# Kernel optimization log

Measured on AMD Instinct MI355X. Metric: run time of the kernel, lower is better.

## Reference

```python
import jax, jax.numpy as jnp
import numpy as np

B, N, C = 32, 2248, 1024
D = 128            # bottleneck (down_size)
P = 200            # num_prompt_tokens
SCALE = D ** (-0.5)


def setup_inputs() -> dict:
    key = jax.random.key(0)
    k = jax.random.split(key, 5)
    return {
        "x": jax.random.normal(k[0], (B, N, C), dtype=jnp.float32),
        "W_down": jax.random.normal(k[1], (C, D), dtype=jnp.float32) * (C ** -0.5),
        "b_down": jax.random.normal(k[2], (D,), dtype=jnp.float32) * 0.01,
        "W_up": jax.random.normal(k[3], (D, C), dtype=jnp.float32) * (D ** -0.5),
        "b_up": jax.random.normal(k[4], (C,), dtype=jnp.float32) * 0.01,
        "gate": jnp.ones((), dtype=jnp.float32),
    }


def reference(x, W_down, b_down, W_up, b_up, gate):
    # down-projection + exact GELU (torch nn.GELU default is erf-based)
    down = jax.nn.gelu(jnp.einsum('bnc,cd->bnd', x, W_down) + b_down,
                       approximate=False)                      # [B, N, D]
    prompt_down = down[:, :P, :]                               # [B, P, D]
    token_down = down[:, P:, :]                                # [B, N-P, D]
    # prompt-token cross attention
    attn = jax.nn.softmax(
        jnp.einsum('bpd,btd->bpt', prompt_down, token_down) * SCALE, axis=-1)
    prompt_out = jnp.einsum('bpt,btd->bpd', attn, token_down)  # [B, P, D]
    combined = jnp.concatenate([prompt_out, token_down], axis=1)  # [B, N, D]
    up = jnp.einsum('bnd,dc->bnc', combined, W_up) + b_up      # [B, N, C]
    return gate * up
```

## Files before the change

### kernel.cpp

```cpp
#include <hip/hip_runtime.h>
#include <hip/hip_bf16.h>
#include <math.h>

#define B_   32
#define N_   2248
#define C_   1024
#define D_   128
#define P_   200
#define T_   2048
#define M_   (B_ * N_)
#define SCALE_ 0.08838834764831845f

typedef __bf16 bf16;
typedef __bf16 bf16x8 __attribute__((ext_vector_type(8)));
typedef __bf16 bf16x4 __attribute__((ext_vector_type(4)));
typedef float  f32x4  __attribute__((ext_vector_type(4)));
typedef unsigned int u32x4 __attribute__((ext_vector_type(4)));

#define VT_COL(dd, t) ((((((t) >> 3) ^ (((dd) >> 3) & 7)) << 3)) | ((t) & 7))

__global__ void k_prep(const float* __restrict__ Wd, const float* __restrict__ Wu,
                       bf16* __restrict__ WtD, bf16* __restrict__ WtU) {
    int i = blockIdx.x * 256 + threadIdx.x;
    if (i >= 131072) return;
    int d = i >> 10, k = i & 1023;
    WtD[i] = (bf16)Wd[k * 128 + d];
    int c = i >> 7, e = i & 127;
    WtU[i] = (bf16)Wu[e * 1024 + c];
}

__launch_bounds__(256, 3)
__global__ void k_down(const float* __restrict__ x, const bf16* __restrict__ WtD,
                       const float* __restrict__ bd, bf16* __restrict__ down) {
    __shared__ bf16 As[2][128][72];
    const int tid = threadIdx.x;
    const int lane = tid & 63, wid = tid >> 6;
    const int wm = wid >> 1, wn = wid & 1;
    const int li = lane & 15, lg = lane >> 4;
    const int m0 = blockIdx.x * 128;
    const bf16* Bp = WtD + (size_t)(wn * 64 + li) * C_ + lg * 8;

    int r_[4], c_[4];
    const float* sp[4];
#pragma unroll
    for (int it = 0; it < 4; it++) {
        int ch = tid + it * 256;
        r_[it] = ch >> 3;
        c_[it] = (ch & 7) * 8;
        sp[it] = x + (size_t)(m0 + r_[it]) * C_ + c_[it];
    }

    f32x4 stg[8];
#pragma unroll
    for (int it = 0; it < 4; it++) {
        stg[2 * it]     = *(const f32x4*)(sp[it]);
        stg[2 * it + 1] = *(const f32x4*)(sp[it] + 4);
    }
#pragma unroll
    for (int it = 0; it < 4; it++) {
        bf16x8 o;
        o[0] = (bf16)stg[2*it][0]; o[1] = (bf16)stg[2*it][1];
        o[2] = (bf16)stg[2*it][2]; o[3] = (bf16)stg[2*it][3];
        o[4] = (bf16)stg[2*it+1][0]; o[5] = (bf16)stg[2*it+1][1];
        o[6] = (bf16)stg[2*it+1][2]; o[7] = (bf16)stg[2*it+1][3];
        *(bf16x8*)&As[0][r_[it]][c_[it]] = o;
    }

    f32x4 acc[4][4];
    const f32x4 zero = {0.f, 0.f, 0.f, 0.f};
#pragma unroll
    for (int i = 0; i < 4; i++)
#pragma unroll
        for (int j = 0; j < 4; j++) acc[i][j] = zero;

    int cur = 0;
    for (int t = 0; t < 16; t++) {
        __syncthreads();
        if (t < 15) {
#pragma unroll
            for (int it = 0; it < 4; it++) {
                stg[2 * it]     = *(const f32x4*)(sp[it] + (t + 1) * 64);
                stg[2 * it + 1] = *(const f32x4*)(sp[it] + (t + 1) * 64 + 4);
            }
        }
        const int k0 = t * 64;
#pragma unroll
        for (int kk = 0; kk < 2; kk++) {
            bf16x8 af[4], bf_[4];
#pragma unroll
            for (int f = 0; f < 4; f++)
                bf_[f] = *(const bf16x8*)(Bp + (size_t)(f * 16) * C_ + k0 + kk * 32);
#pragma unroll
            for (int f = 0; f < 4; f++)
                af[f] = *(const bf16x8*)&As[cur][wm * 64 + f * 16 + li][kk * 32 + lg * 8];
#pragma unroll
            for (int fm = 0; fm < 4; fm++)
#pragma unroll
                for (int fn = 0; fn < 4; fn++)
                    acc[fm][fn] = __builtin_amdgcn_mfma_f32_16x16x32_bf16(
                        af[fm], bf_[fn], acc[fm][fn], 0, 0, 0);
        }
        if (t < 15) {
#pragma unroll
            for (int it = 0; it < 4; it++) {
                bf16x8 o;
                o[0] = (bf16)stg[2*it][0]; o[1] = (bf16)stg[2*it][1];
                o[2] = (bf16)stg[2*it][2]; o[3] = (bf16)stg[2*it][3];
                o[4] = (bf16)stg[2*it+1][0]; o[5] = (bf16)stg[2*it+1][1];
                o[6] = (bf16)stg[2*it+1][2]; o[7] = (bf16)stg[2*it+1][3];
                *(bf16x8*)&As[cur ^ 1][r_[it]][c_[it]] = o;
            }
        }
        cur ^= 1;
    }
#pragma unroll
    for (int fn = 0; fn < 4; fn++) {
        int col = wn * 64 + fn * 16 + li;
        float bias = bd[col];
#pragma unroll
        for (int fm = 0; fm < 4; fm++) {
            int rb = m0 + wm * 64 + fm * 16 + lg * 4;
#pragma unroll
            for (int r = 0; r < 4; r++) {
                float v = acc[fm][fn][r] + bias;
                float g = 0.5f * v * (1.0f + erff(v * 0.70710678118654752f));
                down[(size_t)(rb + r) * D_ + col] = (bf16)g;
            }
        }
    }
}

__launch_bounds__(256, 2)
__global__ void k_attn(const bf16* __restrict__ down, float* __restrict__ Opart,
                       float* __restrict__ Mpart, float* __restrict__ Lpart) {
    __shared__ bf16 Qs[64][136];
    __shared__ bf16 Ks[64][136];
    __shared__ bf16 Vt[128][72];
    __shared__ bf16 Ps[4][16][72];
    const int tid = threadIdx.x;
    const int lane = tid & 63, w = tid >> 6;
    const int li = lane & 15, lg = lane >> 4;
    const int bid = blockIdx.x;
    const int wg = (bid & 7) * 64 + (bid >> 3);
    const int b  = wg >> 4;
    const int qt = (wg >> 2) & 3;
    const int th = wg & 3;
    const size_t base = (size_t)b * N_ * D_;
    const int tbase = P_ + th * 512;

#pragma unroll
    for (int it = 0; it < 4; it++) {
        int ch = tid + it * 256;
        int r = ch >> 4, c8 = (ch & 15) * 8;
        *(u32x4*)&Qs[r][c8] = *(const u32x4*)(down + base + (size_t)(qt * 64 + r) * D_ + c8);
    }
    __syncthreads();
    bf16x8 qf[4];
#pragma unroll
    for (int kk = 0; kk < 4; kk++)
        qf[kk] = *(const bf16x8*)&Qs[w * 16 + li][kk * 32 + lg * 8];

    float m_run[4], l_run[4];
    f32x4 acc[8];
    const f32x4 zero = {0.f, 0.f, 0.f, 0.f};
#pragma unroll
    for (int r = 0; r < 4; r++) { m_run[r] = -3.0e38f; l_run[r] = 0.f; }
#pragma unroll
    for (int fn = 0; fn < 8; fn++) acc[fn] = zero;

    for (int tt = 0; tt < 8; tt++) {
        __syncthreads();
#pragma unroll
        for (int it = 0; it < 4; it++) {
            int ch = tid + it * 256;
            int r = ch >> 4, c8 = (ch & 15) * 8;
            u32x4 v = *(const u32x4*)(down + base + (size_t)(tbase + tt * 64 + r) * D_ + c8);
            *(u32x4*)&Ks[r][c8] = v;
            bf16 tmp[8];
            *(u32x4*)tmp = v;
#pragma unroll
            for (int j = 0; j < 8; j++) Vt[c8 + j][VT_COL(c8 + j, r)] = tmp[j];
        }
        __syncthreads();
        f32x4 s[4];
#pragma unroll
        for (int fn = 0; fn < 4; fn++) {
            s[fn] = zero;
#pragma unroll
            for (int kk = 0; kk < 4; kk++) {
                bf16x8 kf = *(const bf16x8*)&Ks[fn * 16 + li][kk * 32 + lg * 8];
                s[fn] = __builtin_amdgcn_mfma_f32_16x16x32_bf16(qf[kk], kf, s[fn], 0, 0, 0);
            }
            s[fn] *= SCALE_;
        }
#pragma unroll
        for (int r = 0; r < 4; r++) {
            float tmax = fmaxf(fmaxf(s[0][r], s[1][r]), fmaxf(s[2][r], s[3][r]));
#pragma unroll
            for (int off = 1; off < 16; off <<= 1)
                tmax = fmaxf(tmax, __shfl_xor(tmax, off, 64));
            float mnew = fmaxf(m_run[r], tmax);
            float corr = __expf(m_run[r] - mnew);
            m_run[r] = mnew;
            float psum = 0.f;
#pragma unroll
            for (int fn = 0; fn < 4; fn++) {
                float p = __expf(s[fn][r] - mnew);
                psum += p;
                Ps[w][lg * 4 + r][fn * 16 + li] = (bf16)p;
            }
#pragma unroll
            for (int off = 1; off < 16; off <<= 1)
                psum += __shfl_xor(psum, off, 64);
            l_run[r] = l_run[r] * corr + psum;
#pragma unroll
            for (int fn = 0; fn < 8; fn++) acc[fn][r] *= corr;
        }
#pragma unroll
        for (int kk = 0; kk < 2; kk++) {
            bf16x8 pf = *(const bf16x8*)&Ps[w][li][kk * 32 + lg * 8];
#pragma unroll
            for (int fn = 0; fn < 8; fn++) {
                int d = fn * 16 + li;
                bf16x8 vf = *(const bf16x8*)&Vt[d][VT_COL(d, kk * 32 + lg * 8)];
                acc[fn] = __builtin_amdgcn_mfma_f32_16x16x32_bf16(pf, vf, acc[fn], 0, 0, 0);
            }
        }
    }
#pragma unroll
    for (int r = 0; r < 4; r++) {
        int q = qt * 64 + w * 16 + lg * 4 + r;
        size_t ro = ((size_t)(b * 4 + th) * 256 + q) * 128;
#pragma unroll
        for (int fn = 0; fn < 8; fn++)
            Opart[ro + fn * 16 + li] = acc[fn][r];
        if (li == 0) {
            Mpart[(b * 4 + th) * 256 + q] = m_run[r];
            Lpart[(b * 4 + th) * 256 + q] = l_run[r];
        }
    }
}

__global__ void k_comb(const float* __restrict__ Opart, const float* __restrict__ Mpart,
                       const float* __restrict__ Lpart, bf16* __restrict__ pout) {
    int gid = blockIdx.x * 256 + threadIdx.x;
    if (gid >= (B_ * P_ * D_) / 4) return;
    int e = gid * 4;
    int row = e >> 7;
    int col = e & 127;
    int b = row / P_;
    int q = row - b * P_;
    float mm[4], ll[4];
    float m = -3.0e38f;
#pragma unroll
    for (int t = 0; t < 4; t++) {
        mm[t] = Mpart[(b * 4 + t) * 256 + q];
        ll[t] = Lpart[(b * 4 + t) * 256 + q];
        m = fmaxf(m, mm[t]);
    }
    float a[4], lsum = 0.f;
#pragma unroll
    for (int t = 0; t < 4; t++) { a[t] = __expf(mm[t] - m); lsum += ll[t] * a[t]; }
    float inv = 1.0f / lsum;
    f32x4 o = {0.f, 0.f, 0.f, 0.f};
#pragma unroll
    for (int t = 0; t < 4; t++) {
        f32x4 ot = *(const f32x4*)&Opart[((size_t)(b * 4 + t) * 256 + q) * 128 + col];
#pragma unroll
        for (int j = 0; j < 4; j++) o[j] += ot[j] * a[t];
    }
    bf16x4 ob;
#pragma unroll
    for (int j = 0; j < 4; j++) ob[j] = (bf16)(o[j] * inv);
    *(bf16x4*)&pout[(size_t)row * 128 + col] = ob;
}

__launch_bounds__(256, 3)
__global__ void k_up(const bf16* __restrict__ down, const bf16* __restrict__ pout,
                     const bf16* __restrict__ WtU, const float* __restrict__ bu,
                     const float* __restrict__ gate, float* __restrict__ out) {
    const int tid = threadIdx.x;
    const int lane = tid & 63, wid = tid >> 6;
    const int wm = wid >> 1, wn = wid & 1;
    const int li = lane & 15, lg = lane >> 4;
    int bid = blockIdx.x;
    int wg = (bid & 7) * 562 + (bid >> 3);
    const int mt = wg >> 3, nt = wg & 7;
    const int m0 = mt * 128, n0 = nt * 128;

    const bf16* rp[4];
#pragma unroll
    for (int f = 0; f < 4; f++) {
        int row = m0 + wm * 64 + f * 16 + li;
        int bb = row / N_;
        int n = row - bb * N_;
        rp[f] = (n < P_) ? (pout + (size_t)(bb * P_ + n) * D_ + lg * 8)
                         : (down + (size_t)row * D_ + lg * 8);
    }
    const bf16* Bp = WtU + (size_t)(n0 + wn * 64 + li) * D_ + lg * 8;

    f32x4 acc[4][4];
    const f32x4 zero = {0.f, 0.f, 0.f, 0.f};
#pragma unroll
    for (int i = 0; i < 4; i++)
#pragma unroll
        for (int j = 0; j < 4; j++) acc[i][j] = zero;

#pragma unroll
    for (int kk = 0; kk < 4; kk++) {
        bf16x8 af[4], bf_[4];
#pragma unroll
        for (int f = 0; f < 4; f++) {
            af[f]  = *(const bf16x8*)(rp[f] + kk * 32);
            bf_[f] = *(const bf16x8*)(Bp + (size_t)(f * 16) * D_ + kk * 32);
        }
#pragma unroll
        for (int fm = 0; fm < 4; fm++)
#pragma unroll
            for (int fn = 0; fn < 4; fn++)
                acc[fm][fn] = __builtin_amdgcn_mfma_f32_16x16x32_bf16(
                    af[fm], bf_[fn], acc[fm][fn], 0, 0, 0);
    }

    float g = gate[0];
#pragma unroll
    for (int fn = 0; fn < 4; fn++) {
        int c = n0 + wn * 64 + fn * 16 + li;
        float bias = bu[c];
#pragma unroll
        for (int fm = 0; fm < 4; fm++) {
            int rb = m0 + wm * 64 + fm * 16 + lg * 4;
#pragma unroll
            for (int r = 0; r < 4; r++)
                out[(size_t)(rb + r) * C_ + c] = g * (acc[fm][fn][r] + bias);
        }
    }
}

extern "C" void kernel_launch(void* const* d_in, const int* in_sizes, int n_in,
                              void* d_out, int out_size, void* d_ws, size_t ws_size,
                              hipStream_t stream) {
    const float* x    = (const float*)d_in[0];
    const float* Wd   = (const float*)d_in[1];
    const float* bd   = (const float*)d_in[2];
    const float* Wu   = (const float*)d_in[3];
    const float* bu   = (const float*)d_in[4];
    const float* gate = (const float*)d_in[5];
    float* out = (float*)d_out;

    char* w = (char*)d_ws;
    bf16*  down  = (bf16*)w;
    bf16*  pout  = (bf16*)(w + 18415616);
    bf16*  WtD   = (bf16*)(w + 20054016);
    bf16*  WtU   = (bf16*)(w + 20316160);
    float* Opart = (float*)(w + 20578304);
    float* Mpart = (float*)(w + 37355520);
    float* Lpart = (float*)(w + 37486592);

    k_prep<<<512, 256, 0, stream>>>(Wd, Wu, WtD, WtU);
    k_down<<<M_ / 128, 256, 0, stream>>>(x, WtD, bd, down);
    k_attn<<<512, 256, 0, stream>>>(down, Opart, Mpart, Lpart);
    k_comb<<<800, 256, 0, stream>>>(Opart, Mpart, Lpart, pout);
    k_up<<<(M_ / 128) * 8, 256, 0, stream>>>(down, pout, WtU, bu, gate, out);
}
```

Before: 255.7 us.

## Retile down-projection GEMM to 64-row blocks with full-width warp N tiles

The down-projection kernel now uses 64-row M tiles with 128-wide K steps. Each warp owns 16 rows and all 128 output columns, where before a 2x2 warp grid split 64x64 tiles. The change doubles the block count, lowers per-thread accumulator registers, and raises the occupancy hint from 3 to 4. In exchange, each warp now re-reads the whole WtD slice from global/L2 per A fragment, which raises weight traffic per row.

```diff
diff --git a/kernel.cpp b/kernel.cpp
--- a/kernel.cpp
+++ b/kernel.cpp
@@ -29,24 +29,23 @@
     WtU[i] = (bf16)Wu[e * 1024 + c];
 }
 
-__launch_bounds__(256, 3)
+__launch_bounds__(256, 4)
 __global__ void k_down(const float* __restrict__ x, const bf16* __restrict__ WtD,
                        const float* __restrict__ bd, bf16* __restrict__ down) {
-    __shared__ bf16 As[2][128][72];
+    __shared__ bf16 As[2][64][136];
     const int tid = threadIdx.x;
-    const int lane = tid & 63, wid = tid >> 6;
-    const int wm = wid >> 1, wn = wid & 1;
+    const int lane = tid & 63, w = tid >> 6;
     const int li = lane & 15, lg = lane >> 4;
-    const int m0 = blockIdx.x * 128;
-    const bf16* Bp = WtD + (size_t)(wn * 64 + li) * C_ + lg * 8;
+    const int m0 = blockIdx.x * 64;
+    const bf16* Bp = WtD + (size_t)li * C_ + lg * 8;
 
     int r_[4], c_[4];
     const float* sp[4];
 #pragma unroll
     for (int it = 0; it < 4; it++) {
         int ch = tid + it * 256;
-        r_[it] = ch >> 3;
-        c_[it] = (ch & 7) * 8;
+        r_[it] = ch >> 4;
+        c_[it] = (ch & 15) * 8;
         sp[it] = x + (size_t)(m0 + r_[it]) * C_ + c_[it];
     }
 
@@ -59,53 +58,44 @@
 #pragma unroll
     for (int it = 0; it < 4; it++) {
         bf16x8 o;
-        o[0] = (bf16)stg[2*it][0]; o[1] = (bf16)stg[2*it][1];
-        o[2] = (bf16)stg[2*it][2]; o[3] = (bf16)stg[2*it][3];
+        o[0] = (bf16)stg[2*it][0];   o[1] = (bf16)stg[2*it][1];
+        o[2] = (bf16)stg[2*it][2];   o[3] = (bf16)stg[2*it][3];
         o[4] = (bf16)stg[2*it+1][0]; o[5] = (bf16)stg[2*it+1][1];
         o[6] = (bf16)stg[2*it+1][2]; o[7] = (bf16)stg[2*it+1][3];
         *(bf16x8*)&As[0][r_[it]][c_[it]] = o;
     }
 
-    f32x4 acc[4][4];
+    f32x4 acc[8];
     const f32x4 zero = {0.f, 0.f, 0.f, 0.f};
 #pragma unroll
-    for (int i = 0; i < 4; i++)
-#pragma unroll
-        for (int j = 0; j < 4; j++) acc[i][j] = zero;
+    for (int f = 0; f < 8; f++) acc[f] = zero;
 
     int cur = 0;
-    for (int t = 0; t < 16; t++) {
+    for (int t = 0; t < 8; t++) {
         __syncthreads();
-        if (t < 15) {
+        if (t < 7) {
 #pragma unroll
             for (int it = 0; it < 4; it++) {
-                stg[2 * it]     = *(const f32x4*)(sp[it] + (t + 1) * 64);
-                stg[2 * it + 1] = *(const f32x4*)(sp[it] + (t + 1) * 64 + 4);
-            }
-        }
-        const int k0 = t * 64;
-#pragma unroll
-        for (int kk = 0; kk < 2; kk++) {
-            bf16x8 af[4], bf_[4];
-#pragma unroll
-            for (int f = 0; f < 4; f++)
-                bf_[f] = *(const bf16x8*)(Bp + (size_t)(f * 16) * C_ + k0 + kk * 32);
-#pragma unroll
-            for (int f = 0; f < 4; f++)
-                af[f] = *(const bf16x8*)&As[cur][wm * 64 + f * 16 + li][kk * 32 + lg * 8];
-#pragma unroll
-            for (int fm = 0; fm < 4; fm++)
-#pragma unroll
-                for (int fn = 0; fn < 4; fn++)
-                    acc[fm][fn] = __builtin_amdgcn_mfma_f32_16x16x32_bf16(
-                        af[fm], bf_[fn], acc[fm][fn], 0, 0, 0);
-        }
-        if (t < 15) {
+                stg[2 * it]     = *(const f32x4*)(sp[it] + (t + 1) * 128);
+                stg[2 * it + 1] = *(const f32x4*)(sp[it] + (t + 1) * 128 + 4);
+            }
+        }
+        const int k0 = t * 128;
+#pragma unroll
+        for (int kk = 0; kk < 4; kk++) {
+            bf16x8 af = *(const bf16x8*)&As[cur][w * 16 + li][kk * 32 + lg * 8];
+#pragma unroll
+            for (int f = 0; f < 8; f++) {
+                bf16x8 bf_ = *(const bf16x8*)(Bp + (size_t)(f * 16) * C_ + k0 + kk * 32);
+                acc[f] = __builtin_amdgcn_mfma_f32_16x16x32_bf16(af, bf_, acc[f], 0, 0, 0);
+            }
+        }
+        if (t < 7) {
 #pragma unroll
             for (int it = 0; it < 4; it++) {
                 bf16x8 o;
-                o[0] = (bf16)stg[2*it][0]; o[1] = (bf16)stg[2*it][1];
-                o[2] = (bf16)stg[2*it][2]; o[3] = (bf16)stg[2*it][3];
+                o[0] = (bf16)stg[2*it][0];   o[1] = (bf16)stg[2*it][1];
+                o[2] = (bf16)stg[2*it][2];   o[3] = (bf16)stg[2*it][3];
                 o[4] = (bf16)stg[2*it+1][0]; o[5] = (bf16)stg[2*it+1][1];
                 o[6] = (bf16)stg[2*it+1][2]; o[7] = (bf16)stg[2*it+1][3];
                 *(bf16x8*)&As[cur ^ 1][r_[it]][c_[it]] = o;
@@ -114,18 +104,14 @@
         cur ^= 1;
     }
 #pragma unroll
-    for (int fn = 0; fn < 4; fn++) {
-        int col = wn * 64 + fn * 16 + li;
+    for (int f = 0; f < 8; f++) {
+        int col = f * 16 + li;
         float bias = bd[col];
 #pragma unroll
-        for (int fm = 0; fm < 4; fm++) {
-            int rb = m0 + wm * 64 + fm * 16 + lg * 4;
-#pragma unroll
-            for (int r = 0; r < 4; r++) {
-                float v = acc[fm][fn][r] + bias;
-                float g = 0.5f * v * (1.0f + erff(v * 0.70710678118654752f));
-                down[(size_t)(rb + r) * D_ + col] = (bf16)g;
-            }
+        for (int r = 0; r < 4; r++) {
+            float v = acc[f][r] + bias;
+            float g = 0.5f * v * (1.0f + erff(v * 0.70710678118654752f));
+            down[(size_t)(m0 + w * 16 + lg * 4 + r) * D_ + col] = (bf16)g;
         }
     }
 }
@@ -358,7 +344,7 @@
     float* Lpart = (float*)(w + 37486592);
 
     k_prep<<<512, 256, 0, stream>>>(Wd, Wu, WtD, WtU);
-    k_down<<<M_ / 128, 256, 0, stream>>>(x, WtD, bd, down);
+    k_down<<<M_ / 64, 256, 0, stream>>>(x, WtD, bd, down);
     k_attn<<<512, 256, 0, stream>>>(down, Opart, Mpart, Lpart);
     k_comb<<<800, 256, 0, stream>>>(Opart, Mpart, Lpart, pout);
     k_up<<<(M_ / 128) * 8, 256, 0, stream>>>(down, pout, WtU, bu, gate, out);
```

Measured after the change: 371.1 us. +45.1%, slower.
